# Optimization experiments

Hardware: AMD Instinct MI355X
Metric: run time of the kernel (lower is better)

## Reference

```python
import jax, jax.numpy as jnp
import numpy as np

BS, L, NIMG, D, H, DH, V, NL = 16, 256, 256, 512, 8, 256, 1000, 6


def _softmax_one(x):
    # softmax with +1 in denominator (post max-shift, literal +1 as in source)
    m = jnp.max(x, axis=-1, keepdims=True)
    e = jnp.exp(x - m)
    return e / (1.0 + jnp.sum(e, axis=-1, keepdims=True))


def _ln(x, g, b):
    mu = jnp.mean(x, axis=-1, keepdims=True)
    var = jnp.var(x, axis=-1, keepdims=True)
    return (x - mu) * jax.lax.rsqrt(var + 1e-5) * g + b


def _mha(xq, xkv, wq, b_q, wk, b_k, wv, b_v, wo, b_o, mask):
    b, nq, _ = xq.shape
    nk = xkv.shape[1]
    q = (xq @ wq + b_q).reshape(b, nq, H, DH).transpose(0, 2, 1, 3)
    k = (xkv @ wk + b_k).reshape(b, nk, H, DH).transpose(0, 2, 1, 3)
    v = (xkv @ wv + b_v).reshape(b, nk, H, DH).transpose(0, 2, 1, 3)
    s = jnp.einsum('bhqd,bhkd->bhqk', q, k) / jnp.sqrt(jnp.float32(DH))
    if mask is not None:
        s = s + mask[:, None]  # (b,1,nq,nk) additive mask
    o = jnp.einsum('bhqk,bhkd->bhqd', _softmax_one(s), v)
    return o.transpose(0, 2, 1, 3).reshape(b, nq, H * DH) @ wo + b_o


def _forward(program, pro_adj, img_features, embed, W_in, b_in, ln1_g, ln1_b, ln2_g, ln2_b,
             Wq, bq, Wk, bk, Wv, bv, Wo, bo, f_W1, f_b1, f_W2, f_b2,
             cWq, cbq, cWk, cbk, cWv, cbv, cWo, cbo):
    mask = (1.0 - pro_adj.astype(jnp.float32)) * -1e6
    bs, length = program.shape[:2]
    x = embed[program].reshape(bs, length, -1) @ W_in + b_in  # (bs, L, D)
    for i in range(NL):
        # self-attn transformer layer (pre-LN, residual)
        h = _ln(x, ln1_g[i], ln1_b[i])
        x = x + _mha(h, h, Wq[i], bq[i], Wk[i], bk[i], Wv[i], bv[i], Wo[i], bo[i], mask)
        h2 = _ln(x, ln2_g[i], ln2_b[i])
        x = x + (jax.nn.gelu(h2 @ f_W1[i] + f_b1[i], approximate=False) @ f_W2[i] + f_b2[i])
        # cross-modal attention to image features, residual add
        x = x + _mha(x, img_features, cWq[i], cbq[i], cWk[i], cbk[i], cWv[i], cbv[i], cWo[i], cbo[i], None)
    return x


def setup_inputs() -> dict:
    key = jax.random.key(0)
    ks = jax.random.split(key, 16)
    def n(k, shape):
        return jax.random.normal(k, shape, jnp.float32) * 0.02
    program = jax.random.randint(ks[0], (BS, L, 8), 0, V, dtype=jnp.int32)
    pro_adj = jax.random.randint(ks[1], (BS, L, L), 0, 2, dtype=jnp.int32)
    img_features = jax.random.normal(ks[2], (BS, NIMG, D), jnp.float32)
    embed = n(ks[3], (V, 300)).at[0].set(0.0)  # padding_idx=0
    return dict(
        program=program, pro_adj=pro_adj, img_features=img_features, embed=embed,
        W_in=n(ks[4], (8 * 300, D)), b_in=jnp.zeros((D,), jnp.float32),
        ln1_g=jnp.ones((NL, D), jnp.float32), ln1_b=jnp.zeros((NL, D), jnp.float32),
        ln2_g=jnp.ones((NL, D), jnp.float32), ln2_b=jnp.zeros((NL, D), jnp.float32),
        Wq=n(ks[5], (NL, D, H * DH)), bq=jnp.zeros((NL, H * DH), jnp.float32),
        Wk=n(ks[6], (NL, D, H * DH)), bk=jnp.zeros((NL, H * DH), jnp.float32),
        Wv=n(ks[7], (NL, D, H * DH)), bv=jnp.zeros((NL, H * DH), jnp.float32),
        Wo=n(ks[8], (NL, H * DH, D)), bo=jnp.zeros((NL, D), jnp.float32),
        f_W1=n(ks[9], (NL, D, D)), f_b1=jnp.zeros((NL, D), jnp.float32),
        f_W2=n(ks[10], (NL, D, D)), f_b2=jnp.zeros((NL, D), jnp.float32),
        cWq=n(ks[11], (NL, D, H * DH)), cbq=jnp.zeros((NL, H * DH), jnp.float32),
        cWk=n(ks[12], (NL, D, H * DH)), cbk=jnp.zeros((NL, H * DH), jnp.float32),
        cWv=n(ks[13], (NL, D, H * DH)), cbv=jnp.zeros((NL, H * DH), jnp.float32),
        cWo=n(ks[14], (NL, H * DH, D)), cbo=jnp.zeros((NL, D), jnp.float32),
    )


def reference(program, pro_adj, img_features, embed, W_in, b_in, ln1_g, ln1_b, ln2_g, ln2_b,
              Wq, bq, Wk, bk, Wv, bv, Wo, bo, f_W1, f_b1, f_W2, f_b2,
              cWq, cbq, cWk, cbk, cWv, cbv, cWo, cbo):
    return _forward(program, pro_adj, img_features, embed, W_in, b_in, ln1_g, ln1_b, ln2_g, ln2_b,
                    Wq, bq, Wk, bk, Wv, bv, Wo, bo, f_W1, f_b1, f_W2, f_b2,
                    cWq, cbq, cWk, cbk, cWv, cbv, cWo, cbo)
```

## Files before the change

### kernel.cpp

```cpp
#include <hip/hip_runtime.h>
#include <hip/hip_bf16.h>

typedef __attribute__((ext_vector_type(8))) short short8;
typedef __attribute__((ext_vector_type(4))) float f32x4;
typedef unsigned short u16;

__device__ __forceinline__ u16 f2b(float f) {
    unsigned int u = __builtin_bit_cast(unsigned int, f);
    u = u + 0x7fffu + ((u >> 16) & 1u);
    return (u16)(u >> 16);
}

#define EPI_F32      0
#define EPI_RESID_XB 3
#define EPI_GELU     4
#define EPI_KV       7
#define EPI_ATOMIC   9

template<int BM, int BN, int BK, int EPI>
__global__ __launch_bounds__(256, 2) void gemm_bf16(
    const u16* __restrict__ A, long aStride, int lda,
    const u16* __restrict__ B, long bStride, int ldb,
    int M, int N, int K,
    const float* __restrict__ bias0, const float* __restrict__ bias1,
    int biasStride,
    const float* __restrict__ Rsd,
    float* __restrict__ outF, u16* __restrict__ outB,
    u16* __restrict__ outV, long outStride, int ldc)
{
    constexpr int WCOLS = (BM == 32) ? 2 : (BN / 64);
    constexpr int WROWS = 4 / WCOLS;
    constexpr int WM = BM / WROWS;
    constexpr int WN = BN / WCOLS;
    constexpr int MF = WM / 16;
    constexpr int NF = WN / 16;
    constexpr int GR = BK / 8;
    constexpr int AUNITS = BM * GR;
    constexpr int TOTU = (BM + BN) * GR;
    constexpr int UPT = (TOTU + 255) / 256;
    constexpr int BUFE = (BM + BN) * BK;

    __shared__ __align__(16) u16 smem[2 * BUFE];

    const int tid = threadIdx.x;
    const int wave = tid >> 6, lane = tid & 63;
    const int wm = wave / WCOLS, wn = wave % WCOLS;

    const int nwg = gridDim.x * gridDim.y;
    const int bl = blockIdx.y * gridDim.x + blockIdx.x;
    const int wsw = (bl & 7) * (nwg >> 3) + (bl >> 3);
    const int bxs = wsw % gridDim.x, bys = wsw / gridDim.x;

    const int tm = bys * BM, tn = bxs * BN;
    const int bz = blockIdx.z;

    const size_t aOff = (size_t)bz * (size_t)aStride;
    const size_t bOff = (size_t)bz * (size_t)bStride;

    const int lr = lane & 15, kg = lane >> 4;

    auto stage = [&](int buf, int k0) {
#pragma unroll
        for (int i = 0; i < UPT; i++) {
            int u = tid + i * 256;
            if (u < TOTU) {
                u16* dst = smem + buf * BUFE + u * 8;
                bool isA = u < AUNITS;
                int v = isA ? u : u - AUNITS;
                int row, kloc;
                if constexpr (BK == 64) {
                    row = v >> 3;
                    int hh = (v >> 2) & 1, g = v & 3;
                    kloc = ((hh ^ (row & 1)) << 5) + ((g ^ ((row >> 1) & 3)) << 3);
                } else {
                    row = v >> 2;
                    int g = v & 3;
                    kloc = (g ^ ((row >> 1) & 3)) << 3;
                }
                const u16* src = isA
                    ? A + aOff + (size_t)(tm + row) * lda + k0 + kloc
                    : B + bOff + (size_t)(tn + row) * ldb + k0 + kloc;
                __builtin_amdgcn_global_load_lds(src, dst, 16, 0, 0);
            }
        }
    };

    auto ldsOff = [&](int row, int kk) -> int {
        if constexpr (BK == 64)
            return row * 64 + (((kk ^ (row & 1)) * 4 + (kg ^ ((row >> 1) & 3))) * 8);
        else
            return row * 32 + ((kg ^ ((row >> 1) & 3)) * 8);
    };

    f32x4 acc[MF][NF];
#pragma unroll
    for (int m = 0; m < MF; m++)
#pragma unroll
        for (int n = 0; n < NF; n++) acc[m][n] = (f32x4)(0.f);

    const int NT = K / BK;
    stage(0, 0);
    __syncthreads();

    for (int t = 0; t < NT; t++) {
        const int cur = t & 1;
        if (t + 1 < NT) stage(cur ^ 1, (t + 1) * BK);

        const u16* As = smem + cur * BUFE;
        const u16* Bs = As + BM * BK;
#pragma unroll
        for (int kk = 0; kk < BK / 32; kk++) {
            short8 af[MF], bfr[NF];
#pragma unroll
            for (int m = 0; m < MF; m++) {
                int row = wm * WM + m * 16 + lr;
                af[m] = *(const short8*)&As[ldsOff(row, kk)];
            }
#pragma unroll
            for (int n = 0; n < NF; n++) {
                int row = wn * WN + n * 16 + lr;
                bfr[n] = *(const short8*)&Bs[ldsOff(row, kk)];
            }
#pragma unroll
            for (int m = 0; m < MF; m++)
#pragma unroll
                for (int n = 0; n < NF; n++)
                    acc[m][n] = __builtin_amdgcn_mfma_f32_16x16x32_bf16(
                        af[m], bfr[n], acc[m][n], 0, 0, 0);
        }
        __syncthreads();
    }

    if constexpr (EPI == EPI_KV) {
        if (tn < 2048) {
#pragma unroll
            for (int m = 0; m < MF; m++)
#pragma unroll
                for (int n = 0; n < NF; n++)
#pragma unroll
                    for (int e = 0; e < 4; e++) {
                        int r = tm + wm * WM + m * 16 + kg * 4 + e;
                        int c = tn + wn * WN + n * 16 + lr;
                        float t = acc[m][n][e] + bias0[bz * biasStride + c];
                        outB[(size_t)bz * outStride + (size_t)r * 2048 + c] = f2b(t);
                    }
        } else {
            const int ccb = tn - 2048;
            const int bidx = tm >> 8;
            const int hh = ccb >> 8;
            u16* vls = smem;
#pragma unroll
            for (int m = 0; m < MF; m++)
#pragma unroll
                for (int n = 0; n < NF; n++)
#pragma unroll
                    for (int e = 0; e < 4; e++) {
                        int rl = wm * WM + m * 16 + kg * 4 + e;
                        int cl = wn * WN + n * 16 + lr;
                        float t = acc[m][n][e] + bias1[bz * biasStride + ccb + cl];
                        vls[cl * 136 + rl] = f2b(t);
                    }
            __syncthreads();
            const int dloc = tid >> 1;
            const int thalf = (tid & 1) * 64;
            const int dglob = (ccb & 255) + dloc;
            u16* dst = outV + (size_t)bz * outStride +
                       (size_t)(bidx * 8 + hh) * 65536 +
                       (size_t)dglob * 256 + (tm & 255) + thalf;
            const u16* srcl = vls + dloc * 136 + thalf;
#pragma unroll
            for (int k = 0; k < 8; k++)
                *(uint4*)(dst + k * 8) = *(const uint4*)(srcl + k * 8);
        }
        return;
    }

#pragma unroll
    for (int m = 0; m < MF; m++) {
#pragma unroll
        for (int n = 0; n < NF; n++) {
#pragma unroll
            for (int e = 0; e < 4; e++) {
                int r = tm + wm * WM + m * 16 + (lane >> 4) * 4 + e;
                int c = tn + wn * WN + n * 16 + (lane & 15);
                float v = acc[m][n][e];
                if constexpr (EPI == EPI_F32) {
                    outF[(size_t)r * ldc + c] = v + bias0[c];
                } else if constexpr (EPI == EPI_RESID_XB) {
                    float t = v + bias0[c] + Rsd[(size_t)r * ldc + c];
                    outF[(size_t)r * ldc + c] = t;
                    outB[(size_t)r * ldc + c] = f2b(t);
                } else if constexpr (EPI == EPI_GELU) {
                    float t = v + bias0[c];
                    t = 0.5f * t * (1.f + erff(t * 0.70710678118654752f));
                    outB[(size_t)r * ldc + c] = f2b(t);
                } else if constexpr (EPI == EPI_ATOMIC) {
                    float t = v;
                    if (bz == 0) t += bias0[c];
                    atomicAdd(&outF[(size_t)r * ldc + c], t);
                }
            }
        }
    }
}

template<bool MASKED>
__global__ __launch_bounds__(256, 2) void attn_kernel(
    const u16* __restrict__ Aq, const u16* __restrict__ WqT,
    const float* __restrict__ bq,
    const u16* __restrict__ K, const u16* __restrict__ Vt,
    const int* __restrict__ adj, u16* __restrict__ O)
{
    __shared__ __align__(16) u16 Ps[64 * 256];
    __shared__ __align__(16) u16 Ks[2 * 256 * 32];
    __shared__ __align__(16) u16 Aql[2 * 64 * 32];
    __shared__ float red1[64 * 4];
    __shared__ float red2[64 * 4];

    const int tid = threadIdx.x;
    const int w = tid >> 6, lane = tid & 63;
    const int lr = lane & 15, kg = lane >> 4;

    const int nwg = gridDim.x * gridDim.y;
    const int bl = blockIdx.y * gridDim.x + blockIdx.x;
    const int wsw = (bl & 7) * (nwg >> 3) + (bl >> 3);
    const int qt = wsw % gridDim.x, bh = wsw / gridDim.x;

    const int b = bh >> 3, h = bh & 7;
    const size_t qkBase = (size_t)b * 256 * 2048 + h * 256;

    auto stageA0 = [&](int buf, int k0) {
        int u = tid;
        int row = u >> 2, g = u & 3;
        int gs = g ^ ((row >> 1) & 3);
        const u16* src = Aq + (size_t)(b * 256 + qt * 64 + row) * 512 + k0 + gs * 8;
        __builtin_amdgcn_global_load_lds(src, Aql + buf * 2048 + u * 8, 16, 0, 0);
    };
    auto stageB0 = [&](int buf, int k0) {
#pragma unroll
        for (int i = 0; i < 4; i++) {
            int u = tid + i * 256;
            int row = u >> 2, g = u & 3;
            int gs = g ^ ((row >> 1) & 3);
            const u16* src = WqT + (size_t)(h * 256 + row) * 512 + k0 + gs * 8;
            __builtin_amdgcn_global_load_lds(src, Ks + buf * 8192 + u * 8, 16, 0, 0);
        }
    };
    auto stageK = [&](int buf, int dk) {
#pragma unroll
        for (int i = 0; i < 4; i++) {
            int u = w * 256 + i * 64 + lane;
            int row = u >> 2, g = u & 3;
            int gs = g ^ ((row >> 1) & 3);
            const u16* src = K + qkBase + (size_t)row * 2048 + dk * 32 + gs * 8;
            __builtin_amdgcn_global_load_lds(src, Ks + buf * 8192 + u * 8, 16, 0, 0);
        }
    };
    auto stageV = [&](int buf, int kt) {
#pragma unroll
        for (int i = 0; i < 4; i++) {
            int u = w * 256 + i * 64 + lane;
            int row = u >> 2, g = u & 3;
            int gs = g ^ ((row >> 1) & 3);
            const u16* src = Vt + (size_t)bh * 65536 + (size_t)row * 256 + kt * 32 + gs * 8;
            __builtin_amdgcn_global_load_lds(src, Ks + buf * 8192 + u * 8, 16, 0, 0);
        }
    };

    {
        f32x4 qacc[4][4];
#pragma unroll
        for (int m = 0; m < 4; m++)
#pragma unroll
            for (int n = 0; n < 4; n++) qacc[m][n] = (f32x4)(0.f);

        stageA0(0, 0);
        stageB0(0, 0);
        __syncthreads();
        for (int t = 0; t < 16; t++) {
            const int cur = t & 1;
            if (t < 15) { stageA0(cur ^ 1, (t + 1) * 32); stageB0(cur ^ 1, (t + 1) * 32); }
            short8 af[4], bfr[4];
#pragma unroll
            for (int m = 0; m < 4; m++) {
                int row = m * 16 + lr;
                af[m] = *(const short8*)&Aql[cur * 2048 + row * 32 + ((kg ^ ((row >> 1) & 3)) * 8)];
            }
#pragma unroll
            for (int n = 0; n < 4; n++) {
                int row = w * 64 + n * 16 + lr;
                bfr[n] = *(const short8*)&Ks[cur * 8192 + row * 32 + ((kg ^ ((row >> 1) & 3)) * 8)];
            }
            __builtin_amdgcn_s_setprio(1);
#pragma unroll
            for (int m = 0; m < 4; m++)
#pragma unroll
                for (int n = 0; n < 4; n++)
                    qacc[m][n] = __builtin_amdgcn_mfma_f32_16x16x32_bf16(
                        af[m], bfr[n], qacc[m][n], 0, 0, 0);
            __builtin_amdgcn_s_setprio(0);
            __syncthreads();
        }
        stageK(0, 0);
#pragma unroll
        for (int m = 0; m < 4; m++)
#pragma unroll
            for (int n = 0; n < 4; n++)
#pragma unroll
                for (int e = 0; e < 4; e++) {
                    int q = m * 16 + kg * 4 + e;
                    int d = w * 64 + n * 16 + lr;
                    float t = qacc[m][n][e] + bq[h * 256 + d];
                    Ps[q * 256 + (((d >> 3) ^ (q & 7)) * 8) + (d & 7)] = f2b(t);
                }
    }
    __syncthreads();

    f32x4 sacc[4][4];
#pragma unroll
    for (int m = 0; m < 4; m++)
#pragma unroll
        for (int n = 0; n < 4; n++) sacc[m][n] = (f32x4)(0.f);

    for (int dk = 0; dk < 8; dk++) {
        const int cur = dk & 1;
        if (dk < 7) {
            stageK(cur ^ 1, dk + 1);
            asm volatile("s_waitcnt vmcnt(4)" ::: "memory");
        } else {
            asm volatile("s_waitcnt vmcnt(0)" ::: "memory");
        }
        __builtin_amdgcn_sched_barrier(0);
        short8 af[4], bfr[4];
#pragma unroll
        for (int m = 0; m < 4; m++) {
            int row = m * 16 + lr;
            af[m] = *(const short8*)&Ps[row * 256 + (((dk * 4 + kg) ^ (row & 7)) * 8)];
        }
#pragma unroll
        for (int n = 0; n < 4; n++) {
            int row = w * 64 + n * 16 + lr;
            bfr[n] = *(const short8*)&Ks[cur * 8192 + row * 32 + ((kg ^ ((row >> 1) & 3)) * 8)];
        }
        __builtin_amdgcn_s_setprio(1);
#pragma unroll
        for (int m = 0; m < 4; m++)
#pragma unroll
            for (int n = 0; n < 4; n++)
                sacc[m][n] = __builtin_amdgcn_mfma_f32_16x16x32_bf16(
                    af[m], bfr[n], sacc[m][n], 0, 0, 0);
        __builtin_amdgcn_s_setprio(0);
    }

    stageV(0, 0);

#pragma unroll
    for (int m = 0; m < 4; m++)
#pragma unroll
        for (int n = 0; n < 4; n++)
#pragma unroll
            for (int e = 0; e < 4; e++) {
                float t = sacc[m][n][e] * 0.0625f;
                if (MASKED) {
                    int q = qt * 64 + m * 16 + kg * 4 + e;
                    int k = w * 64 + n * 16 + lr;
                    int a_ = adj[((size_t)b * 256 + q) * 256 + k];
                    t += (1.f - (float)a_) * -1.0e6f;
                }
                sacc[m][n][e] = t;
            }

    float mx[4][4];
#pragma unroll
    for (int m = 0; m < 4; m++)
#pragma unroll
        for (int e = 0; e < 4; e++) {
            float v = sacc[m][0][e];
#pragma unroll
            for (int n = 1; n < 4; n++) v = fmaxf(v, sacc[m][n][e]);
#pragma unroll
            for (int off = 1; off < 16; off <<= 1) v = fmaxf(v, __shfl_xor(v, off));
            mx[m][e] = v;
        }
    if (lr == 0) {
#pragma unroll
        for (int m = 0; m < 4; m++)
#pragma unroll
            for (int e = 0; e < 4; e++)
                red1[(m * 16 + kg * 4 + e) * 4 + w] = mx[m][e];
    }
    __syncthreads();

    float inv[4][4];
    float sum[4][4];
#pragma unroll
    for (int m = 0; m < 4; m++)
#pragma unroll
        for (int e = 0; e < 4; e++) {
            int r = m * 16 + kg * 4 + e;
            float gm = fmaxf(fmaxf(red1[r * 4 + 0], red1[r * 4 + 1]),
                             fmaxf(red1[r * 4 + 2], red1[r * 4 + 3]));
            float s = 0.f;
#pragma unroll
            for (int n = 0; n < 4; n++) {
                float ev = __expf(sacc[m][n][e] - gm);
                sacc[m][n][e] = ev;
                s += ev;
            }
            sum[m][e] = s;
        }
#pragma unroll
    for (int m = 0; m < 4; m++)
#pragma unroll
        for (int e = 0; e < 4; e++) {
            float s = sum[m][e];
#pragma unroll
            for (int off = 1; off < 16; off <<= 1) s += __shfl_xor(s, off);
            sum[m][e] = s;
        }
    if (lr == 0) {
#pragma unroll
        for (int m = 0; m < 4; m++)
#pragma unroll
            for (int e = 0; e < 4; e++)
                red2[(m * 16 + kg * 4 + e) * 4 + w] = sum[m][e];
    }
    __syncthreads();
#pragma unroll
    for (int m = 0; m < 4; m++)
#pragma unroll
        for (int e = 0; e < 4; e++) {
            int r = m * 16 + kg * 4 + e;
            float gs = red2[r * 4 + 0] + red2[r * 4 + 1] +
                       red2[r * 4 + 2] + red2[r * 4 + 3];
            inv[m][e] = 1.f / (1.f + gs);
        }

#pragma unroll
    for (int m = 0; m < 4; m++)
#pragma unroll
        for (int n = 0; n < 4; n++)
#pragma unroll
            for (int e = 0; e < 4; e++) {
                int q = m * 16 + kg * 4 + e;
                int k = w * 64 + n * 16 + lr;
                float pv = sacc[m][n][e] * inv[m][e];
                Ps[q * 256 + (((k >> 3) ^ (q & 7)) * 8) + (k & 7)] = f2b(pv);
            }
    __syncthreads();

    f32x4 oacc[4][4];
#pragma unroll
    for (int m = 0; m < 4; m++)
#pragma unroll
        for (int n = 0; n < 4; n++) oacc[m][n] = (f32x4)(0.f);

    for (int kt = 0; kt < 8; kt++) {
        const int cur = kt & 1;
        if (kt < 7) {
            stageV(cur ^ 1, kt + 1);
            asm volatile("s_waitcnt vmcnt(4)" ::: "memory");
        } else {
            asm volatile("s_waitcnt vmcnt(0)" ::: "memory");
        }
        __builtin_amdgcn_sched_barrier(0);
        short8 af[4], bfr[4];
#pragma unroll
        for (int m = 0; m < 4; m++) {
            int q = m * 16 + lr;
            af[m] = *(const short8*)&Ps[q * 256 + (((kt * 4 + kg) ^ (q & 7)) * 8)];
        }
#pragma unroll
        for (int n = 0; n < 4; n++) {
            int row = w * 64 + n * 16 + lr;
            bfr[n] = *(const short8*)&Ks[cur * 8192 + row * 32 + ((kg ^ ((row >> 1) & 3)) * 8)];
        }
        __builtin_amdgcn_s_setprio(1);
#pragma unroll
        for (int m = 0; m < 4; m++)
#pragma unroll
            for (int n = 0; n < 4; n++)
                oacc[m][n] = __builtin_amdgcn_mfma_f32_16x16x32_bf16(
                    af[m], bfr[n], oacc[m][n], 0, 0, 0);
        __builtin_amdgcn_s_setprio(0);
    }

#pragma unroll
    for (int m = 0; m < 4; m++)
#pragma unroll
        for (int n = 0; n < 4; n++)
#pragma unroll
            for (int e = 0; e < 4; e++) {
                int q = qt * 64 + m * 16 + kg * 4 + e;
                int d = w * 64 + n * 16 + lr;
                O[(size_t)(b * 256 + q) * 2048 + h * 256 + d] = f2b(oacc[m][n][e]);
            }
}

__global__ __launch_bounds__(256) void transpose_kernel(
    const float* p0, const float* p1, const float* p2,
    const float* p3, const float* p4, const float* p5,
    int nsrc, long srcLayerStride, int R, int C,
    u16* __restrict__ out, long dstMatStride, long dstLayerStride)
{
    const int mat = blockIdx.z % nsrc, layer = blockIdx.z / nsrc;
    const float* W;
    switch (mat) {
    default: W = p0; break;
    case 1: W = p1; break;
    case 2: W = p2; break;
    case 3: W = p3; break;
    case 4: W = p4; break;
    case 5: W = p5; break;
    }
    W += (size_t)layer * srcLayerStride;
    u16* o = out + (size_t)layer * dstLayerStride + (size_t)mat * dstMatStride;
    __shared__ float t[64][65];
    const int tid = threadIdx.x;
    const int rBase = blockIdx.y * 64, cBase = blockIdx.x * 64;
#pragma unroll
    for (int i = 0; i < 4; i++) {
        int idx = tid + i * 256;
        int rr = idx >> 4, cc4 = (idx & 15) * 4;
        if (rBase + rr < R) {
            float4 v = *(const float4*)&W[(size_t)(rBase + rr) * C + cBase + cc4];
            t[rr][cc4] = v.x; t[rr][cc4 + 1] = v.y;
            t[rr][cc4 + 2] = v.z; t[rr][cc4 + 3] = v.w;
        }
    }
    __syncthreads();
#pragma unroll
    for (int i = 0; i < 4; i++) {
        int idx = tid + i * 256;
        int cc = idx >> 4, rr4 = (idx & 15) * 4;
        if (rBase + rr4 < R) {
            uint2 pk;
            pk.x = (unsigned)f2b(t[rr4][cc]) | ((unsigned)f2b(t[rr4 + 1][cc]) << 16);
            pk.y = (unsigned)f2b(t[rr4 + 2][cc]) | ((unsigned)f2b(t[rr4 + 3][cc]) << 16);
            *(uint2*)&o[(size_t)(cBase + cc) * R + rBase + rr4] = pk;
        }
    }
}

__global__ __launch_bounds__(256) void ln_kernel(
    const float* __restrict__ X, const float* __restrict__ g,
    const float* __restrict__ b, u16* __restrict__ Y)
{
    const int wave = threadIdx.x >> 6, lane = threadIdx.x & 63;
    const size_t row = (size_t)blockIdx.x * 4 + wave;
    const float* xr = X + row * 512;
    float4 v0 = *reinterpret_cast<const float4*>(xr + lane * 8);
    float4 v1 = *reinterpret_cast<const float4*>(xr + lane * 8 + 4);
    float s = v0.x + v0.y + v0.z + v0.w + v1.x + v1.y + v1.z + v1.w;
    float ss = v0.x * v0.x + v0.y * v0.y + v0.z * v0.z + v0.w * v0.w +
               v1.x * v1.x + v1.y * v1.y + v1.z * v1.z + v1.w * v1.w;
#pragma unroll
    for (int off = 32; off; off >>= 1) {
        s += __shfl_xor(s, off);
        ss += __shfl_xor(ss, off);
    }
    float mu = s * (1.0f / 512.0f);
    float var = ss * (1.0f / 512.0f) - mu * mu;
    float rs = rsqrtf(var + 1e-5f);
    float4 g0 = *reinterpret_cast<const float4*>(g + lane * 8);
    float4 g1 = *reinterpret_cast<const float4*>(g + lane * 8 + 4);
    float4 b0 = *reinterpret_cast<const float4*>(b + lane * 8);
    float4 b1 = *reinterpret_cast<const float4*>(b + lane * 8 + 4);
    float o0 = (v0.x - mu) * rs * g0.x + b0.x;
    float o1 = (v0.y - mu) * rs * g0.y + b0.y;
    float o2 = (v0.z - mu) * rs * g0.z + b0.z;
    float o3 = (v0.w - mu) * rs * g0.w + b0.w;
    float o4 = (v1.x - mu) * rs * g1.x + b1.x;
    float o5 = (v1.y - mu) * rs * g1.y + b1.y;
    float o6 = (v1.z - mu) * rs * g1.z + b1.z;
    float o7 = (v1.w - mu) * rs * g1.w + b1.w;
    uint4 pk;
    pk.x = (unsigned)f2b(o0) | ((unsigned)f2b(o1) << 16);
    pk.y = (unsigned)f2b(o2) | ((unsigned)f2b(o3) << 16);
    pk.z = (unsigned)f2b(o4) | ((unsigned)f2b(o5) << 16);
    pk.w = (unsigned)f2b(o6) | ((unsigned)f2b(o7) << 16);
    *reinterpret_cast<uint4*>(Y + row * 512 + lane * 8) = pk;
}

__global__ __launch_bounds__(256) void gather_kernel(
    const int* __restrict__ program, const float* __restrict__ embed,
    unsigned* __restrict__ Ag2, int total2)
{
    int idx = blockIdx.x * 256 + threadIdx.x;
    if (idx >= total2) return;
    int t = idx / 1200;
    int rem = idx - t * 1200;
    int j = rem / 150;
    int e2 = rem - j * 150;
    int tok = program[t * 8 + j];
    float2 v = *reinterpret_cast<const float2*>(&embed[(size_t)tok * 300 + e2 * 2]);
    Ag2[idx] = (unsigned)f2b(v.x) | ((unsigned)f2b(v.y) << 16);
}

__global__ __launch_bounds__(256) void cvt_kernel(
    const float* __restrict__ in, u16* __restrict__ out, int n4)
{
    int i = blockIdx.x * 256 + threadIdx.x;
    if (i >= n4) return;
    float4 v = reinterpret_cast<const float4*>(in)[i];
    uint2 pk;
    pk.x = (unsigned)f2b(v.x) | ((unsigned)f2b(v.y) << 16);
    pk.y = (unsigned)f2b(v.z) | ((unsigned)f2b(v.w) << 16);
    reinterpret_cast<uint2*>(out)[i] = pk;
}


extern "C" void kernel_launch(void* const* d_in, const int* in_sizes, int n_in,
                              void* d_out, int out_size, void* d_ws, size_t ws_size,
                              hipStream_t stream)
{
    const int*   program = (const int*)d_in[0];
    const int*   adj     = (const int*)d_in[1];
    const float* img     = (const float*)d_in[2];
    const float* embed   = (const float*)d_in[3];
    const float* W_in    = (const float*)d_in[4];
    const float* b_in    = (const float*)d_in[5];
    const float* ln1_g   = (const float*)d_in[6];
    const float* ln1_b   = (const float*)d_in[7];
    const float* ln2_g   = (const float*)d_in[8];
    const float* ln2_b   = (const float*)d_in[9];
    const float* Wq      = (const float*)d_in[10];
    const float* bq      = (const float*)d_in[11];
    const float* Wk      = (const float*)d_in[12];
    const float* bk      = (const float*)d_in[13];
    const float* Wv      = (const float*)d_in[14];
    const float* bv      = (const float*)d_in[15];
    const float* Wo      = (const float*)d_in[16];
    const float* bo      = (const float*)d_in[17];
    const float* fW1     = (const float*)d_in[18];
    const float* fb1     = (const float*)d_in[19];
    const float* fW2     = (const float*)d_in[20];
    const float* fb2     = (const float*)d_in[21];
    const float* cWq     = (const float*)d_in[22];
    const float* cbq     = (const float*)d_in[23];
    const float* cWk     = (const float*)d_in[24];
    const float* cbk     = (const float*)d_in[25];
    const float* cWv     = (const float*)d_in[26];
    const float* cbv     = (const float*)d_in[27];
    const float* cWo     = (const float*)d_in[28];
    const float* cbo     = (const float*)d_in[29];

    char* wsb = (char*)d_ws;
    const size_t MB = 1024 * 1024;
    const long Mi = 1048576;
    const long LSTR = 8 * Mi + Mi / 2;

    float* x    = (float*)(wsb + 0);
    u16*   h    = (u16*)(wsb + 8 * MB);
    u16*   xb   = (u16*)(wsb + 12 * MB);
    u16*   imgb = (u16*)(wsb + 16 * MB);
    u16*   WinT = (u16*)(wsb + 20 * MB);
    u16*   Kb   = (u16*)(wsb + 24 * MB);
    u16*   Vt   = (u16*)(wsb + 40 * MB);
    u16*   O    = (u16*)(wsb + 56 * MB);
    u16*   Wall = (u16*)(wsb + 72 * MB);
    u16*   KcA  = (u16*)(wsb + 176 * MB);
    u16*   VcA  = (u16*)(wsb + 272 * MB);
    u16*   Ag   = Kb;
    u16*   g    = Kb;

    const bool bigws = ws_size >= (size_t)175 * MB;
    const bool hoist = ws_size >= (size_t)369 * MB && bigws;

    gather_kernel<<<19200, 256, 0, stream>>>(program, embed, (unsigned*)Ag, 4915200);
    transpose_kernel<<<dim3(8, 38, 1), 256, 0, stream>>>(
        W_in, nullptr, nullptr, nullptr, nullptr, nullptr,
        1, 0, 2400, 512, WinT, 0, 0);
    cvt_kernel<<<2048, 256, 0, stream>>>(img, imgb, 524288);
    if (bigws) {
        transpose_kernel<<<dim3(32, 8, 36), 256, 0, stream>>>(
            Wq, Wk, Wv, cWq, cWk, cWv, 6, Mi, 512, 2048, Wall, Mi, LSTR);
        transpose_kernel<<<dim3(8, 32, 12), 256, 0, stream>>>(
            Wo, cWo, nullptr, nullptr, nullptr, nullptr,
            2, Mi, 2048, 512, Wall + 6 * Mi, Mi, LSTR);
        transpose_kernel<<<dim3(8, 8, 12), 256, 0, stream>>>(
            fW1, fW2, nullptr, nullptr, nullptr, nullptr,
            2, 262144, 512, 512, Wall + 8 * Mi, 262144, LSTR);
    }
    gemm_bf16<64, 64, 32, EPI_F32><<<dim3(8, 64, 1), 256, 0, stream>>>(
        Ag, 0, 2400, WinT, 0, 2400, 4096, 512, 2400,
        b_in, nullptr, 0, nullptr,
        x, nullptr, nullptr, 0, 512);
    if (hoist) {
        gemm_bf16<128, 128, 64, EPI_KV><<<dim3(32, 32, 6), 256, 0, stream>>>(
            imgb, 0, 512, Wall + 4 * Mi, LSTR, 512, 4096, 4096, 512,
            cbk, cbv, 2048, nullptr,
            nullptr, KcA, VcA, 8 * Mi, 2048);
    }

    for (int l = 0; l < 6; l++) {
        u16* Wl = Wall + (bigws ? (size_t)l * LSTR : 0);
        if (!bigws) {
            transpose_kernel<<<dim3(32, 8, 6), 256, 0, stream>>>(
                Wq + (size_t)l * Mi, Wk + (size_t)l * Mi, Wv + (size_t)l * Mi,
                cWq + (size_t)l * Mi, cWk + (size_t)l * Mi, cWv + (size_t)l * Mi,
                6, 0, 512, 2048, Wl, Mi, 0);
            transpose_kernel<<<dim3(8, 32, 2), 256, 0, stream>>>(
                Wo + (size_t)l * Mi, cWo + (size_t)l * Mi,
                nullptr, nullptr, nullptr, nullptr,
                2, 0, 2048, 512, Wl + 6 * Mi, Mi, 0);
            transpose_kernel<<<dim3(8, 8, 2), 256, 0, stream>>>(
                fW1 + (size_t)l * 262144, fW2 + (size_t)l * 262144,
                nullptr, nullptr, nullptr, nullptr,
                2, 0, 512, 512, Wl + 8 * Mi, 262144, 0);
        }

        ln_kernel<<<1024, 256, 0, stream>>>(x, ln1_g + l * 512, ln1_b + l * 512, h);
        gemm_bf16<128, 128, 64, EPI_KV><<<dim3(32, 32, 1), 256, 0, stream>>>(
            h, 0, 512, Wl + 1 * Mi, 0, 512, 4096, 4096, 512,
            bk + l * 2048, bv + l * 2048, 0, nullptr,
            nullptr, Kb, Vt, 0, 2048);
        attn_kernel<true><<<dim3(4, 128), 256, 0, stream>>>(
            h, Wl, bq + l * 2048, Kb, Vt, adj, O);
        gemm_bf16<64, 64, 64, EPI_ATOMIC><<<dim3(8, 64, 2), 256, 0, stream>>>(
            O, 1024, 2048, Wl + 6 * Mi, 1024, 2048, 4096, 512, 1024,
            bo + l * 512, nullptr, 0, nullptr,
            x, nullptr, nullptr, 0, 512);

        ln_kernel<<<1024, 256, 0, stream>>>(x, ln2_g + l * 512, ln2_b + l * 512, h);
        gemm_bf16<64, 64, 64, EPI_GELU><<<dim3(8, 64, 1), 256, 0, stream>>>(
            h, 0, 512, Wl + 8 * Mi, 0, 512, 4096, 512, 512,
            fb1 + l * 512, nullptr, 0, nullptr,
            nullptr, g, nullptr, 0, 512);
        gemm_bf16<64, 64, 64, EPI_RESID_XB><<<dim3(8, 64, 1), 256, 0, stream>>>(
            g, 0, 512, Wl + 8 * Mi + 262144, 0, 512, 4096, 512, 512,
            fb2 + l * 512, nullptr, 0, x,
            x, xb, nullptr, 0, 512);

        u16* Kc = hoist ? (KcA + (size_t)l * 8 * Mi) : Kb;
        u16* Vc = hoist ? (VcA + (size_t)l * 8 * Mi) : Vt;
        if (!hoist) {
            gemm_bf16<128, 128, 64, EPI_KV><<<dim3(32, 32, 1), 256, 0, stream>>>(
                imgb, 0, 512, Wl + 4 * Mi, 0, 512, 4096, 4096, 512,
                cbk + l * 2048, cbv + l * 2048, 0, nullptr,
                nullptr, Kb, Vt, 0, 2048);
        }
        attn_kernel<false><<<dim3(4, 128), 256, 0, stream>>>(
            xb, Wl + 3 * Mi, cbq + l * 2048, Kc, Vc, nullptr, O);
        gemm_bf16<64, 64, 64, EPI_ATOMIC><<<dim3(8, 64, 2), 256, 0, stream>>>(
            O, 1024, 2048, Wl + 7 * Mi, 1024, 2048, 4096, 512, 1024,
            cbo + l * 512, nullptr, 0, nullptr,
            x, nullptr, nullptr, 0, 512);
    }

    hipMemcpyAsync(d_out, x, (size_t)2097152 * sizeof(float),
                   hipMemcpyDeviceToDevice, stream);
}
```

Baseline: 1.341 ms.

## Triple-buffer GEMM LDS pipeline, shrink KV tile, widen transpose blocks

The bf16 GEMM moves from double to triple buffering, keeping two K-tiles of global-to-LDS loads in flight and syncing with explicit vmcnt waits and raw barriers instead of a full __syncthreads per iteration. The K/V projection GEMMs switch from 128x128 to 128x64 tiles on twice as many workgroups, and the V-transpose epilogue is remapped to match. The weight transpose kernel now handles 128 rows per block and issues all its loads before any LDS writes. The changes target load latency in the GEMM main loop and occupancy on the KV GEMMs. In exchange they use more LDS per block, and the UPT change assumes the tile's load units divide evenly by 256.

```diff
diff --git a/kernel.cpp b/kernel.cpp
--- a/kernel.cpp
+++ b/kernel.cpp
@@ -9,6 +9,15 @@
     unsigned int u = __builtin_bit_cast(unsigned int, f);
     u = u + 0x7fffu + ((u >> 16) & 1u);
     return (u16)(u >> 16);
+}
+
+template<int N> __device__ __forceinline__ void vmwait() {
+    if constexpr (N == 0)       asm volatile("s_waitcnt vmcnt(0)" ::: "memory");
+    else if constexpr (N == 2)  asm volatile("s_waitcnt vmcnt(2)" ::: "memory");
+    else if constexpr (N == 4)  asm volatile("s_waitcnt vmcnt(4)" ::: "memory");
+    else if constexpr (N == 6)  asm volatile("s_waitcnt vmcnt(6)" ::: "memory");
+    else if constexpr (N == 8)  asm volatile("s_waitcnt vmcnt(8)" ::: "memory");
+    else                        asm volatile("s_waitcnt vmcnt(12)" ::: "memory");
 }
 
 #define EPI_F32      0
@@ -37,10 +46,10 @@
     constexpr int GR = BK / 8;
     constexpr int AUNITS = BM * GR;
     constexpr int TOTU = (BM + BN) * GR;
-    constexpr int UPT = (TOTU + 255) / 256;
+    constexpr int UPT = TOTU / 256;
     constexpr int BUFE = (BM + BN) * BK;
 
-    __shared__ __align__(16) u16 smem[2 * BUFE];
+    __shared__ __align__(16) u16 smem[3 * BUFE];
 
     const int tid = threadIdx.x;
     const int wave = tid >> 6, lane = tid & 63;
@@ -63,25 +72,23 @@
 #pragma unroll
         for (int i = 0; i < UPT; i++) {
             int u = tid + i * 256;
-            if (u < TOTU) {
-                u16* dst = smem + buf * BUFE + u * 8;
-                bool isA = u < AUNITS;
-                int v = isA ? u : u - AUNITS;
-                int row, kloc;
-                if constexpr (BK == 64) {
-                    row = v >> 3;
-                    int hh = (v >> 2) & 1, g = v & 3;
-                    kloc = ((hh ^ (row & 1)) << 5) + ((g ^ ((row >> 1) & 3)) << 3);
-                } else {
-                    row = v >> 2;
-                    int g = v & 3;
-                    kloc = (g ^ ((row >> 1) & 3)) << 3;
-                }
-                const u16* src = isA
-                    ? A + aOff + (size_t)(tm + row) * lda + k0 + kloc
-                    : B + bOff + (size_t)(tn + row) * ldb + k0 + kloc;
-                __builtin_amdgcn_global_load_lds(src, dst, 16, 0, 0);
-            }
+            u16* dst = smem + buf * BUFE + u * 8;
+            bool isA = u < AUNITS;
+            int v = isA ? u : u - AUNITS;
+            int row, kloc;
+            if constexpr (BK == 64) {
+                row = v >> 3;
+                int hh = (v >> 2) & 1, g = v & 3;
+                kloc = ((hh ^ (row & 1)) << 5) + ((g ^ ((row >> 1) & 3)) << 3);
+            } else {
+                row = v >> 2;
+                int g = v & 3;
+                kloc = (g ^ ((row >> 1) & 3)) << 3;
+            }
+            const u16* src = isA
+                ? A + aOff + (size_t)(tm + row) * lda + k0 + kloc
+                : B + bOff + (size_t)(tn + row) * ldb + k0 + kloc;
+            __builtin_amdgcn_global_load_lds(src, dst, 16, 0, 0);
         }
     };
 
@@ -100,11 +107,17 @@
 
     const int NT = K / BK;
     stage(0, 0);
-    __syncthreads();
+    if (NT > 1) stage(1, BK);
 
     for (int t = 0; t < NT; t++) {
-        const int cur = t & 1;
-        if (t + 1 < NT) stage(cur ^ 1, (t + 1) * BK);
+        const int cur = t % 3;
+        __builtin_amdgcn_s_barrier();
+        if (t + 2 < NT) stage((t + 2) % 3, (t + 2) * BK);
+        if (t + 2 < NT)      vmwait<2 * UPT>();
+        else if (t + 1 < NT) vmwait<UPT>();
+        else                 vmwait<0>();
+        __builtin_amdgcn_sched_barrier(0);
+        __builtin_amdgcn_s_barrier();
 
         const u16* As = smem + cur * BUFE;
         const u16* Bs = As + BM * BK;
@@ -128,10 +141,10 @@
                     acc[m][n] = __builtin_amdgcn_mfma_f32_16x16x32_bf16(
                         af[m], bfr[n], acc[m][n], 0, 0, 0);
         }
+    }
+
+    if constexpr (EPI == EPI_KV) {
         __syncthreads();
-    }
-
-    if constexpr (EPI == EPI_KV) {
         if (tn < 2048) {
 #pragma unroll
             for (int m = 0; m < MF; m++)
@@ -161,15 +174,15 @@
                         vls[cl * 136 + rl] = f2b(t);
                     }
             __syncthreads();
-            const int dloc = tid >> 1;
-            const int thalf = (tid & 1) * 64;
+            const int dloc = tid >> 2;
+            const int toff = (tid & 3) * 32;
             const int dglob = (ccb & 255) + dloc;
             u16* dst = outV + (size_t)bz * outStride +
                        (size_t)(bidx * 8 + hh) * 65536 +
-                       (size_t)dglob * 256 + (tm & 255) + thalf;
-            const u16* srcl = vls + dloc * 136 + thalf;
-#pragma unroll
-            for (int k = 0; k < 8; k++)
+                       (size_t)dglob * 256 + (tm & 255) + toff;
+            const u16* srcl = vls + dloc * 136 + toff;
+#pragma unroll
+            for (int k = 0; k < 4; k++)
                 *(uint4*)(dst + k * 8) = *(const uint4*)(srcl + k * 8);
         }
         return;
@@ -515,31 +528,47 @@
     }
     W += (size_t)layer * srcLayerStride;
     u16* o = out + (size_t)layer * dstLayerStride + (size_t)mat * dstMatStride;
-    __shared__ float t[64][65];
+    __shared__ float t[2][64][65];
     const int tid = threadIdx.x;
-    const int rBase = blockIdx.y * 64, cBase = blockIdx.x * 64;
-#pragma unroll
-    for (int i = 0; i < 4; i++) {
-        int idx = tid + i * 256;
-        int rr = idx >> 4, cc4 = (idx & 15) * 4;
-        if (rBase + rr < R) {
-            float4 v = *(const float4*)&W[(size_t)(rBase + rr) * C + cBase + cc4];
-            t[rr][cc4] = v.x; t[rr][cc4 + 1] = v.y;
-            t[rr][cc4 + 2] = v.z; t[rr][cc4 + 3] = v.w;
-        }
-    }
+    const int rBase = blockIdx.y * 128, cBase = blockIdx.x * 64;
+
+    float4 va[2][4];
+#pragma unroll
+    for (int tt = 0; tt < 2; tt++)
+#pragma unroll
+        for (int i = 0; i < 4; i++) {
+            int idx = tid + i * 256;
+            int rr = idx >> 4, cc4 = (idx & 15) * 4;
+            int rg = rBase + tt * 64 + rr;
+            va[tt][i] = (rg < R) ? *(const float4*)&W[(size_t)rg * C + cBase + cc4]
+                                 : float4{0.f, 0.f, 0.f, 0.f};
+        }
+#pragma unroll
+    for (int tt = 0; tt < 2; tt++)
+#pragma unroll
+        for (int i = 0; i < 4; i++) {
+            int idx = tid + i * 256;
+            int rr = idx >> 4, cc4 = (idx & 15) * 4;
+            t[tt][rr][cc4]     = va[tt][i].x;
+            t[tt][rr][cc4 + 1] = va[tt][i].y;
+            t[tt][rr][cc4 + 2] = va[tt][i].z;
+            t[tt][rr][cc4 + 3] = va[tt][i].w;
+        }
     __syncthreads();
 #pragma unroll
-    for (int i = 0; i < 4; i++) {
-        int idx = tid + i * 256;
-        int cc = idx >> 4, rr4 = (idx & 15) * 4;
-        if (rBase + rr4 < R) {
-            uint2 pk;
-            pk.x = (unsigned)f2b(t[rr4][cc]) | ((unsigned)f2b(t[rr4 + 1][cc]) << 16);
-            pk.y = (unsigned)f2b(t[rr4 + 2][cc]) | ((unsigned)f2b(t[rr4 + 3][cc]) << 16);
-            *(uint2*)&o[(size_t)(cBase + cc) * R + rBase + rr4] = pk;
-        }
-    }
+    for (int tt = 0; tt < 2; tt++)
+#pragma unroll
+        for (int i = 0; i < 4; i++) {
+            int idx = tid + i * 256;
+            int cc = idx >> 4, rr4 = (idx & 15) * 4;
+            int rg = rBase + tt * 64 + rr4;
+            if (rg < R) {
+                uint2 pk;
+                pk.x = (unsigned)f2b(t[tt][rr4][cc]) | ((unsigned)f2b(t[tt][rr4 + 1][cc]) << 16);
+                pk.y = (unsigned)f2b(t[tt][rr4 + 2][cc]) | ((unsigned)f2b(t[tt][rr4 + 3][cc]) << 16);
+                *(uint2*)&o[(size_t)(cBase + cc) * R + rg] = pk;
+            }
+        }
 }
 
 __global__ __launch_bounds__(256) void ln_kernel(
@@ -668,17 +697,17 @@
     const bool hoist = ws_size >= (size_t)369 * MB && bigws;
 
     gather_kernel<<<19200, 256, 0, stream>>>(program, embed, (unsigned*)Ag, 4915200);
-    transpose_kernel<<<dim3(8, 38, 1), 256, 0, stream>>>(
+    transpose_kernel<<<dim3(8, 19, 1), 256, 0, stream>>>(
         W_in, nullptr, nullptr, nullptr, nullptr, nullptr,
         1, 0, 2400, 512, WinT, 0, 0);
     cvt_kernel<<<2048, 256, 0, stream>>>(img, imgb, 524288);
     if (bigws) {
-        transpose_kernel<<<dim3(32, 8, 36), 256, 0, stream>>>(
+        transpose_kernel<<<dim3(32, 4, 36), 256, 0, stream>>>(
             Wq, Wk, Wv, cWq, cWk, cWv, 6, Mi, 512, 2048, Wall, Mi, LSTR);
-        transpose_kernel<<<dim3(8, 32, 12), 256, 0, stream>>>(
+        transpose_kernel<<<dim3(8, 16, 12), 256, 0, stream>>>(
             Wo, cWo, nullptr, nullptr, nullptr, nullptr,
             2, Mi, 2048, 512, Wall + 6 * Mi, Mi, LSTR);
-        transpose_kernel<<<dim3(8, 8, 12), 256, 0, stream>>>(
+        transpose_kernel<<<dim3(8, 4, 12), 256, 0, stream>>>(
             fW1, fW2, nullptr, nullptr, nullptr, nullptr,
             2, 262144, 512, 512, Wall + 8 * Mi, 262144, LSTR);
     }
@@ -687,7 +716,7 @@
         b_in, nullptr, 0, nullptr,
         x, nullptr, nullptr, 0, 512);
     if (hoist) {
-        gemm_bf16<128, 128, 64, EPI_KV><<<dim3(32, 32, 6), 256, 0, stream>>>(
+        gemm_bf16<128, 64, 64, EPI_KV><<<dim3(64, 32, 6), 256, 0, stream>>>(
             imgb, 0, 512, Wall + 4 * Mi, LSTR, 512, 4096, 4096, 512,
             cbk, cbv, 2048, nullptr,
             nullptr, KcA, VcA, 8 * Mi, 2048);
@@ -696,22 +725,22 @@
     for (int l = 0; l < 6; l++) {
         u16* Wl = Wall + (bigws ? (size_t)l * LSTR : 0);
         if (!bigws) {
-            transpose_kernel<<<dim3(32, 8, 6), 256, 0, stream>>>(
+            transpose_kernel<<<dim3(32, 4, 6), 256, 0, stream>>>(
                 Wq + (size_t)l * Mi, Wk + (size_t)l * Mi, Wv + (size_t)l * Mi,
                 cWq + (size_t)l * Mi, cWk + (size_t)l * Mi, cWv + (size_t)l * Mi,
                 6, 0, 512, 2048, Wl, Mi, 0);
-            transpose_kernel<<<dim3(8, 32, 2), 256, 0, stream>>>(
+            transpose_kernel<<<dim3(8, 16, 2), 256, 0, stream>>>(
                 Wo + (size_t)l * Mi, cWo + (size_t)l * Mi,
                 nullptr, nullptr, nullptr, nullptr,
                 2, 0, 2048, 512, Wl + 6 * Mi, Mi, 0);
-            transpose_kernel<<<dim3(8, 8, 2), 256, 0, stream>>>(
+            transpose_kernel<<<dim3(8, 4, 2), 256, 0, stream>>>(
                 fW1 + (size_t)l * 262144, fW2 + (size_t)l * 262144,
                 nullptr, nullptr, nullptr, nullptr,
                 2, 0, 512, 512, Wl + 8 * Mi, 262144, 0);
         }
 
         ln_kernel<<<1024, 256, 0, stream>>>(x, ln1_g + l * 512, ln1_b + l * 512, h);
-        gemm_bf16<128, 128, 64, EPI_KV><<<dim3(32, 32, 1), 256, 0, stream>>>(
+        gemm_bf16<128, 64, 64, EPI_KV><<<dim3(64, 32, 1), 256, 0, stream>>>(
             h, 0, 512, Wl + 1 * Mi, 0, 512, 4096, 4096, 512,
             bk + l * 2048, bv + l * 2048, 0, nullptr,
             nullptr, Kb, Vt, 0, 2048);
@@ -735,7 +764,7 @@
         u16* Kc = hoist ? (KcA + (size_t)l * 8 * Mi) : Kb;
         u16* Vc = hoist ? (VcA + (size_t)l * 8 * Mi) : Vt;
         if (!hoist) {
-            gemm_bf16<128, 128, 64, EPI_KV><<<dim3(32, 32, 1), 256, 0, stream>>>(
+            gemm_bf16<128, 64, 64, EPI_KV><<<dim3(64, 32, 1), 256, 0, stream>>>(
                 imgb, 0, 512, Wl + 4 * Mi, 0, 512, 4096, 4096, 512,
                 cbk + l * 2048, cbv + l * 2048, 0, nullptr,
                 nullptr, Kb, Vt, 0, 2048);
```

Result: slower. 1.385 ms (+3.3%).
